# Optimization experiments

Measured on AMD Instinct MI355X. Metric: run time of the kernel, lower is better.

Reference implementation:

```python
import jax, jax.numpy as jnp
import numpy as np

MAX_NEIGHBORS = 64  # static cap; >> observed max (~50) for n=9225 uniform pts, r=0.03


def setup_inputs() -> dict:
    key = jax.random.key(0)
    k1, k2 = jax.random.split(key)
    n_batch, n, m, d = 8, 9225, 4096, 2
    data = jax.random.uniform(k1, (n_batch, n, d), dtype=jnp.float32)
    queries = jax.random.uniform(k2, (n_batch, m, d), dtype=jnp.float32)
    radius = jnp.float32(0.03)
    return {"data": data, "queries": queries, "radius": radius}


def reference(data, queries, radius):
    # Faithful JAX translation of native_neighbor_search (use_open3d=False),
    # computed in one shot instead of q_chunk loops (same math), with a static
    # neighbor cap MAX_NEIGHBORS standing in for the data-dependent max.
    B, n, d = data.shape
    m = queries.shape[1]
    # Squared Euclidean distances via the GEMM expansion (equiv. to cdist<=r).
    qn = jnp.sum(queries * queries, axis=-1)              # [B, m]
    dn = jnp.sum(data * data, axis=-1)                    # [B, n]
    cross = jnp.einsum("bmd,bnd->bmn", queries, data)    # [B, m, n]
    sqd = jnp.maximum(qn[:, :, None] + dn[:, None, :] - 2.0 * cross, 0.0)
    in_nbr = sqd <= radius * radius                       # [B, m, n] bool
    counts = jnp.sum(in_nbr, axis=2).astype(jnp.int32)    # [B, m]
    idx = jnp.arange(n, dtype=jnp.int32)                  # [n]
    # invalid slots -> sentinel n, sort compacts valid indices to the front
    valid = jnp.where(in_nbr, idx[None, None, :], jnp.int32(n))
    sorted_idx = jnp.sort(valid, axis=2)[:, :, :MAX_NEIGHBORS]
    neighbors_index = jnp.where(sorted_idx == n, jnp.int32(-1), sorted_idx)
    neighbors_row_splits = jnp.concatenate(
        [jnp.zeros((B, 1), dtype=jnp.int32), jnp.cumsum(counts, axis=1)], axis=1
    )
    return neighbors_index, neighbors_row_splits
```

## Files before the change

### kernel.cpp

```cpp
#include <hip/hip_runtime.h>

#define BATCH 8
#define NPTS 9225
#define MQ 4096
#define CAP 64
#define GRID 32
#define NCELLS (GRID * GRID)

__device__ __forceinline__ int cell_of(float x, float y) {
  int cx = (int)(x * (float)GRID);
  int cy = (int)(y * (float)GRID);
  cx = min(max(cx, 0), GRID - 1);
  cy = min(max(cy, 0), GRID - 1);
  return cy * GRID + cx;
}

__global__ __launch_bounds__(1024) void build_kernel(
    const float* __restrict__ data,
    int* __restrict__ cell_starts,
    float2* __restrict__ sdata, int* __restrict__ sidx) {
  __shared__ int hist[NCELLS];
  __shared__ int cursor[NCELLS];
  const int b = blockIdx.x;
  const int t = threadIdx.x;
  hist[t] = 0;
  __syncthreads();

  const float2* dp = (const float2*)data + (size_t)b * NPTS;
  for (int i = t; i < NPTS; i += 1024)
    atomicAdd(&hist[cell_of(dp[i].x, dp[i].y)], 1);
  __syncthreads();

  const int v = hist[t];
  for (int off = 1; off < NCELLS; off <<= 1) {
    const int u = (t >= off) ? hist[t - off] : 0;
    __syncthreads();
    hist[t] += u;
    __syncthreads();
  }
  const int incl = hist[t];
  const int excl = incl - v;
  cursor[t] = excl;
  cell_starts[b * (NCELLS + 1) + t] = excl;
  if (t == NCELLS - 1) cell_starts[b * (NCELLS + 1) + NCELLS] = incl;
  __syncthreads();

  float2* sd = sdata + (size_t)b * NPTS;
  int* si = sidx + (size_t)b * NPTS;
  for (int i = t; i < NPTS; i += 1024) {
    const float2 p = dp[i];
    const int pos = atomicAdd(&cursor[cell_of(p.x, p.y)], 1);
    sd[pos] = p;
    si[pos] = i;
  }
}

__global__ __launch_bounds__(256) void search_kernel(
    const float* __restrict__ queries, const float* __restrict__ radius_p,
    const int* __restrict__ cell_starts, const float2* __restrict__ sdata,
    const int* __restrict__ sidx, int* __restrict__ nbr_idx,
    int* __restrict__ counts) {
#pragma clang fp contract(off)
  __shared__ int hitbuf[4][CAP];
  const int lane = threadIdx.x & 63;
  const int w = threadIdx.x >> 6;
  const int q = blockIdx.x * 4 + w;
  const int b = q >> 12;
  const float r = radius_p[0];
  const float r2 = r * r;
  const float2 qv = ((const float2*)queries)[q];
  const float qx = qv.x, qy = qv.y;
  const float qn = qx * qx + qy * qy;

  const int cx = min(max((int)(qx * (float)GRID), 0), GRID - 1);
  const int cy = min(max((int)(qy * (float)GRID), 0), GRID - 1);
  const int x0 = max(cx - 1, 0), x1 = min(cx + 1, GRID - 1);
  const int y0 = max(cy - 1, 0), y1 = min(cy + 1, GRID - 1);

  const int csbase = b * (NCELLS + 1);
  int rstart[3], rlen[3];
  int nr = 0;
  for (int y = y0; y <= y1; ++y) {
    const int s0 = cell_starts[csbase + y * GRID + x0];
    const int s1 = cell_starts[csbase + y * GRID + x1 + 1];
    rstart[nr] = s0;
    rlen[nr] = s1 - s0;
    ++nr;
  }
  for (int k = nr; k < 3; ++k) { rstart[k] = 0; rlen[k] = 0; }
  const int L0 = rlen[0];
  const int L01 = L0 + rlen[1];
  const int T = L01 + rlen[2];

  const unsigned long long below = (1ull << lane) - 1ull;
  const float2* sd = sdata + (size_t)b * NPTS;
  const int* si = sidx + (size_t)b * NPTS;
  int h = 0;

  for (int base = 0; base < T; base += 64) {
    const int p = base + lane;
    const bool act = (p < T);
    int i;
    if (p < L0)        i = rstart[0] + p;
    else if (p < L01)  i = rstart[1] + (p - L0);
    else               i = rstart[2] + (p - L01);
    if (!act) i = 0;
    const float2 pt = sd[i];
    const int id = si[i];
    const float dx = pt.x, dy = pt.y;
    const float dn = dx * dx + dy * dy;
    const float cross = qx * dx + qy * dy;
    const float s = (qn + dn) - 2.0f * cross;
    const bool in = act && (s <= r2);
    const unsigned long long mask = __ballot(in);
    if (mask != 0ull) {
      if (in) {
        const int pos = h + __popcll(mask & below);
        if (pos < CAP) hitbuf[w][pos] = id;
      }
      h += __popcll(mask);
    }
  }

  int v = (lane < h && lane < CAP) ? hitbuf[w][lane] : 0x7fffffff;

#pragma unroll
  for (int k = 2; k <= 32; k <<= 1) {
#pragma unroll
    for (int j = k >> 1; j >= 1; j >>= 1) {
      const int other = __shfl_xor(v, j, 64);
      const bool keep_min = (((lane & k) == 0) == ((lane & j) == 0));
      v = keep_min ? min(v, other) : max(v, other);
    }
  }
  if (h > 32) {
#pragma unroll
    for (int j = 32; j >= 1; j >>= 1) {
      const int other = __shfl_xor(v, j, 64);
      const bool keep_min = ((lane & j) == 0);
      v = keep_min ? min(v, other) : max(v, other);
    }
  }

  nbr_idx[(size_t)q * CAP + lane] = (v == 0x7fffffff) ? -1 : v;
  if (lane == 0) counts[q] = h;
}

__global__ __launch_bounds__(256) void scan_kernel(const int* __restrict__ counts,
                                                   int* __restrict__ row_splits) {
  const int b = blockIdx.x;
  const int t = threadIdx.x;
  const int PER = MQ / 256;
  __shared__ int partial[256];
  const int* c = counts + b * MQ;
  int local[PER];
  int sum = 0;
#pragma unroll
  for (int k = 0; k < PER; ++k) { local[k] = c[t * PER + k]; sum += local[k]; }
  partial[t] = sum;
  __syncthreads();
  for (int off = 1; off < 256; off <<= 1) {
    int u = (t >= off) ? partial[t - off] : 0;
    __syncthreads();
    partial[t] += u;
    __syncthreads();
  }
  const int excl = (t == 0) ? 0 : partial[t - 1];
  int* rs = row_splits + b * (MQ + 1);
  if (t == 0) rs[0] = 0;
  int run = excl;
#pragma unroll
  for (int k = 0; k < PER; ++k) { run += local[k]; rs[t * PER + k + 1] = run; }
}

extern "C" void kernel_launch(void* const* d_in, const int* in_sizes, int n_in,
                              void* d_out, int out_size, void* d_ws, size_t ws_size,
                              hipStream_t stream) {
  const float* data    = (const float*)d_in[0];
  const float* queries = (const float*)d_in[1];
  const float* radius  = (const float*)d_in[2];
  int* out        = (int*)d_out;
  int* nbr_idx    = out;
  int* row_splits = out + BATCH * MQ * CAP;

  int* counts      = (int*)d_ws;
  int* cell_starts = counts + BATCH * MQ;
  int* sidx        = cell_starts + BATCH * (NCELLS + 1);
  float2* sdata    = (float2*)(sidx + BATCH * NPTS + 2);

  hipLaunchKernelGGL(build_kernel, dim3(BATCH), dim3(1024), 0, stream,
                     data, cell_starts, sdata, sidx);
  hipLaunchKernelGGL(search_kernel, dim3(BATCH * MQ / 4), dim3(256), 0, stream,
                     queries, radius, cell_starts, sdata, sidx, nbr_idx, counts);
  hipLaunchKernelGGL(scan_kernel, dim3(BATCH), dim3(256), 0, stream,
                     counts, row_splits);
}
```

Baseline: 95.27 us.

## Refine spatial grid to 64x64, pack point records, use wave-scan in build

The uniform grid doubles in resolution to 64x64 and each query now scans a 5x5 cell neighbourhood. The candidate area is smaller, so most queries should fit in about one 64-lane wavefront iteration instead of two. Point coordinates and original indices are packed into one float4 record, so the search loads one 16-byte value instead of two separate arrays. The build kernel's 1024-step block-wide Hillis-Steele scan becomes a per-thread 4-cell sum plus a wavefront shuffle scan, which cuts barriers. In exchange the record is wider (16 bytes per point) and the search juggles five row segments instead of three.

```diff
diff --git a/kernel.cpp b/kernel.cpp
--- a/kernel.cpp
+++ b/kernel.cpp
@@ -4,7 +4,7 @@
 #define NPTS 9225
 #define MQ 4096
 #define CAP 64
-#define GRID 32
+#define GRID 64
 #define NCELLS (GRID * GRID)
 
 __device__ __forceinline__ int cell_of(float x, float y) {
@@ -18,12 +18,14 @@
 __global__ __launch_bounds__(1024) void build_kernel(
     const float* __restrict__ data,
     int* __restrict__ cell_starts,
-    float2* __restrict__ sdata, int* __restrict__ sidx) {
+    float4* __restrict__ recs) {
   __shared__ int hist[NCELLS];
   __shared__ int cursor[NCELLS];
+  __shared__ int wavesum[16];
   const int b = blockIdx.x;
   const int t = threadIdx.x;
-  hist[t] = 0;
+#pragma unroll
+  for (int k = 0; k < NCELLS / 1024; ++k) hist[t + k * 1024] = 0;
   __syncthreads();
 
   const float2* dp = (const float2*)data + (size_t)b * NPTS;
@@ -31,35 +33,41 @@
     atomicAdd(&hist[cell_of(dp[i].x, dp[i].y)], 1);
   __syncthreads();
 
-  const int v = hist[t];
-  for (int off = 1; off < NCELLS; off <<= 1) {
-    const int u = (t >= off) ? hist[t - off] : 0;
-    __syncthreads();
-    hist[t] += u;
-    __syncthreads();
-  }
-  const int incl = hist[t];
-  const int excl = incl - v;
-  cursor[t] = excl;
-  cell_starts[b * (NCELLS + 1) + t] = excl;
-  if (t == NCELLS - 1) cell_starts[b * (NCELLS + 1) + NCELLS] = incl;
-  __syncthreads();
-
-  float2* sd = sdata + (size_t)b * NPTS;
-  int* si = sidx + (size_t)b * NPTS;
+  const int c0 = hist[4 * t + 0], c1 = hist[4 * t + 1];
+  const int c2 = hist[4 * t + 2], c3 = hist[4 * t + 3];
+  const int s = c0 + c1 + c2 + c3;
+  const int lane = t & 63, wid = t >> 6;
+  int v = s;
+#pragma unroll
+  for (int off = 1; off < 64; off <<= 1) {
+    const int u = __shfl_up(v, off, 64);
+    if (lane >= off) v += u;
+  }
+  if (lane == 63) wavesum[wid] = v;
+  __syncthreads();
+  int woff = 0;
+  for (int k = 0; k < wid; ++k) woff += wavesum[k];
+  int e = woff + v - s;
+  int* cs = cell_starts + b * (NCELLS + 1);
+  cs[4 * t + 0] = e; cursor[4 * t + 0] = e; e += c0;
+  cs[4 * t + 1] = e; cursor[4 * t + 1] = e; e += c1;
+  cs[4 * t + 2] = e; cursor[4 * t + 2] = e; e += c2;
+  cs[4 * t + 3] = e; cursor[4 * t + 3] = e; e += c3;
+  if (t == 1023) cs[NCELLS] = e;
+  __syncthreads();
+
+  float4* rb = recs + (size_t)b * NPTS;
   for (int i = t; i < NPTS; i += 1024) {
     const float2 p = dp[i];
     const int pos = atomicAdd(&cursor[cell_of(p.x, p.y)], 1);
-    sd[pos] = p;
-    si[pos] = i;
+    rb[pos] = make_float4(p.x, p.y, __int_as_float(i), 0.0f);
   }
 }
 
 __global__ __launch_bounds__(256) void search_kernel(
     const float* __restrict__ queries, const float* __restrict__ radius_p,
-    const int* __restrict__ cell_starts, const float2* __restrict__ sdata,
-    const int* __restrict__ sidx, int* __restrict__ nbr_idx,
-    int* __restrict__ counts) {
+    const int* __restrict__ cell_starts, const float4* __restrict__ recs,
+    int* __restrict__ nbr_idx, int* __restrict__ counts) {
 #pragma clang fp contract(off)
   __shared__ int hitbuf[4][CAP];
   const int lane = threadIdx.x & 63;
@@ -74,11 +82,11 @@
 
   const int cx = min(max((int)(qx * (float)GRID), 0), GRID - 1);
   const int cy = min(max((int)(qy * (float)GRID), 0), GRID - 1);
-  const int x0 = max(cx - 1, 0), x1 = min(cx + 1, GRID - 1);
-  const int y0 = max(cy - 1, 0), y1 = min(cy + 1, GRID - 1);
+  const int x0 = max(cx - 2, 0), x1 = min(cx + 2, GRID - 1);
+  const int y0 = max(cy - 2, 0), y1 = min(cy + 2, GRID - 1);
 
   const int csbase = b * (NCELLS + 1);
-  int rstart[3], rlen[3];
+  int rstart[5], rlen[5];
   int nr = 0;
   for (int y = y0; y <= y1; ++y) {
     const int s0 = cell_starts[csbase + y * GRID + x0];
@@ -87,39 +95,40 @@
     rlen[nr] = s1 - s0;
     ++nr;
   }
-  for (int k = nr; k < 3; ++k) { rstart[k] = 0; rlen[k] = 0; }
+  for (int k = nr; k < 5; ++k) { rstart[k] = 0; rlen[k] = 0; }
   const int L0 = rlen[0];
-  const int L01 = L0 + rlen[1];
-  const int T = L01 + rlen[2];
+  const int L1 = L0 + rlen[1];
+  const int L2 = L1 + rlen[2];
+  const int L3 = L2 + rlen[3];
+  const int T = L3 + rlen[4];
 
   const unsigned long long below = (1ull << lane) - 1ull;
-  const float2* sd = sdata + (size_t)b * NPTS;
-  const int* si = sidx + (size_t)b * NPTS;
+  const float4* rb = recs + (size_t)b * NPTS;
   int h = 0;
 
   for (int base = 0; base < T; base += 64) {
     const int p = base + lane;
     const bool act = (p < T);
     int i;
-    if (p < L0)        i = rstart[0] + p;
-    else if (p < L01)  i = rstart[1] + (p - L0);
-    else               i = rstart[2] + (p - L01);
+    if (p < L0)      i = rstart[0] + p;
+    else if (p < L1) i = rstart[1] + (p - L0);
+    else if (p < L2) i = rstart[2] + (p - L1);
+    else if (p < L3) i = rstart[3] + (p - L2);
+    else             i = rstart[4] + (p - L3);
     if (!act) i = 0;
-    const float2 pt = sd[i];
-    const int id = si[i];
-    const float dx = pt.x, dy = pt.y;
+    const float4 rec = rb[i];
+    const float dx = rec.x, dy = rec.y;
+    const int id = __float_as_int(rec.z);
     const float dn = dx * dx + dy * dy;
     const float cross = qx * dx + qy * dy;
     const float s = (qn + dn) - 2.0f * cross;
     const bool in = act && (s <= r2);
     const unsigned long long mask = __ballot(in);
-    if (mask != 0ull) {
-      if (in) {
-        const int pos = h + __popcll(mask & below);
-        if (pos < CAP) hitbuf[w][pos] = id;
-      }
-      h += __popcll(mask);
+    if (in) {
+      const int pos = h + __popcll(mask & below);
+      if (pos < CAP) hitbuf[w][pos] = id;
     }
+    h += __popcll(mask);
   }
 
   int v = (lane < h && lane < CAP) ? hitbuf[w][lane] : 0x7fffffff;
@@ -185,13 +194,12 @@
 
   int* counts      = (int*)d_ws;
   int* cell_starts = counts + BATCH * MQ;
-  int* sidx        = cell_starts + BATCH * (NCELLS + 1);
-  float2* sdata    = (float2*)(sidx + BATCH * NPTS + 2);
+  float4* recs     = (float4*)(cell_starts + BATCH * (NCELLS + 1));
 
   hipLaunchKernelGGL(build_kernel, dim3(BATCH), dim3(1024), 0, stream,
-                     data, cell_starts, sdata, sidx);
+                     data, cell_starts, recs);
   hipLaunchKernelGGL(search_kernel, dim3(BATCH * MQ / 4), dim3(256), 0, stream,
-                     queries, radius, cell_starts, sdata, sidx, nbr_idx, counts);
+                     queries, radius, cell_starts, recs, nbr_idx, counts);
   hipLaunchKernelGGL(scan_kernel, dim3(BATCH), dim3(256), 0, stream,
                      counts, row_splits);
 }
```

Measured after the change: 91.29 us. 4.2% less time.
